# Kernel tuning notes

Measured on AMD Instinct MI355X. Metric: run time of the kernel, lower is better.

## Reference

```python
import jax, jax.numpy as jnp
import numpy as np

NW, NT, ND = 100000, 20000, 5000      # wallet / token / dev node counts
DW, DT, DD = 32, 32, 16               # raw feature dims
H = 64                                 # GATConv out channels (heads=1)
E_WW, E_BU, E_SE, E_CR = 1600000, 1000000, 1000000, 20000


def setup_inputs() -> dict:
    key = jax.random.key(0)
    ks = iter(jax.random.split(key, 80))

    def nrm(shape, s=1.0):
        return jax.random.normal(next(ks), shape, dtype=jnp.float32) * s

    inp = {
        "x_wallet": nrm((NW, DW)),
        "x_token": nrm((NT, DT)),
        "x_dev": nrm((ND, DD)),
    }
    # per-relation GATConv params: lin_src, lin_dst (bias=False), att_src, att_dst, bias
    rels = [("g1ww", DW, DW), ("g1bu", DW, DT), ("g1se", DW, DT), ("g1cr", DD, DT),
            ("g2ww", H, H), ("g2bu", H, H), ("g2se", H, H)]
    for pre, ds, dd in rels:
        inp[pre + "_Ws"] = nrm((ds, H), 0.1)
        inp[pre + "_Wd"] = nrm((dd, H), 0.1)
        inp[pre + "_as"] = nrm((H,), 0.1)
        inp[pre + "_ad"] = nrm((H,), 0.1)
        inp[pre + "_b"] = nrm((H,), 0.1)
    inp["Wfc"] = nrm((H, 2), 0.1)
    inp["bfc"] = nrm((2,), 0.1)

    for name, n, hi in [("ww_src", E_WW, NW), ("ww_dst", E_WW, NW),
                        ("bu_src", E_BU, NW), ("bu_dst", E_BU, NT),
                        ("se_src", E_SE, NW), ("se_dst", E_SE, NT),
                        ("cr_src", E_CR, ND), ("cr_dst", E_CR, NT)]:
        inp[name] = jax.random.randint(next(ks), (n,), 0, hi, dtype=jnp.int32)
    return inp


def gat(xs, xd, src, dst, Ws, Wd, a_s, a_d, b, n_dst):
    """PyG GATConv, heads=1, add_self_loops=False, negative_slope=0.2."""
    hs = xs @ Ws                                   # [Ns, H]
    e = jax.nn.leaky_relu((hs @ a_s)[src] + ((xd @ Wd) @ a_d)[dst], 0.2)  # [E]
    m = jax.ops.segment_max(e, dst, num_segments=n_dst)
    ex = jnp.exp(e - m[dst])
    den = jax.ops.segment_sum(ex, dst, num_segments=n_dst)
    alpha = ex / (den[dst] + 1e-16)                # scatter-softmax over dst
    out = jax.ops.segment_sum(alpha[:, None] * hs[src], dst, num_segments=n_dst)
    return out + b


def reference(x_wallet, x_token, x_dev,
              g1ww_Ws, g1ww_Wd, g1ww_as, g1ww_ad, g1ww_b,
              g1bu_Ws, g1bu_Wd, g1bu_as, g1bu_ad, g1bu_b,
              g1se_Ws, g1se_Wd, g1se_as, g1se_ad, g1se_b,
              g1cr_Ws, g1cr_Wd, g1cr_as, g1cr_ad, g1cr_b,
              g2ww_Ws, g2ww_Wd, g2ww_as, g2ww_ad, g2ww_b,
              g2bu_Ws, g2bu_Wd, g2bu_as, g2bu_ad, g2bu_b,
              g2se_Ws, g2se_Wd, g2se_as, g2se_ad, g2se_b,
              Wfc, bfc,
              ww_src, ww_dst, bu_src, bu_dst, se_src, se_dst, cr_src, cr_dst):
    # conv1 (HeteroConv, aggr='sum'): dev has no incoming edges -> dropped
    w1 = gat(x_wallet, x_wallet, ww_src, ww_dst, g1ww_Ws, g1ww_Wd, g1ww_as, g1ww_ad, g1ww_b, NW)
    t1 = (gat(x_wallet, x_token, bu_src, bu_dst, g1bu_Ws, g1bu_Wd, g1bu_as, g1bu_ad, g1bu_b, NT)
          + gat(x_wallet, x_token, se_src, se_dst, g1se_Ws, g1se_Wd, g1se_as, g1se_ad, g1se_b, NT)
          + gat(x_dev, x_token, cr_src, cr_dst, g1cr_Ws, g1cr_Wd, g1cr_as, g1cr_ad, g1cr_b, NT))
    # conv2: 'dev' absent from x_dict, so ('dev','creates','token') is skipped by HeteroConv
    w2 = gat(w1, w1, ww_src, ww_dst, g2ww_Ws, g2ww_Wd, g2ww_as, g2ww_ad, g2ww_b, NW)  # computed but unused downstream (matches torch)
    t2 = (gat(w1, t1, bu_src, bu_dst, g2bu_Ws, g2bu_Wd, g2bu_as, g2bu_ad, g2bu_b, NT)
          + gat(w1, t1, se_src, se_dst, g2se_Ws, g2se_Wd, g2se_as, g2se_ad, g2se_b, NT))
    del w2
    return t2 @ Wfc + bfc  # [NT, 2]
```

## Files before the change

kernel.cpp:

```cpp
#include <hip/hip_runtime.h>

#define NW 100000
#define NT 20000
#define ND 5000
#define EWW 1600000
#define EBU 1000000
#define ESE 1000000
#define ECR 20000
#define EPB 16384
#define BTH 512

#define WWSH 8
#define WWW 256
#define NBWB 391
#define WCAP 6144
#define TSH 6
#define TW 64
#define NBTB 313
#define TCAP 4096
#define CCAP 512

typedef unsigned int uint;

#define R_EDWW 0
#define R_EDBU 1
#define R_EDSE 2
#define R_EDCR 3
#define R_WV2BU 4
#define R_WV2SE 5
#define R_ESWW 6
#define R_ESBU 7
#define R_ESSE 8
#define R_ESCR 9
#define R_WS2BU 10
#define R_WS2SE 11
#define R_VBU 12
#define R_VSE 13
#define R_DBU_B 14
#define R_DSE_B 15
#define R_DBU_S 16
#define R_DSE_S 17
#define R_DBU_C 18
#define R_DSE_C 19
#define R_TBU0 20
#define R_TBU1 21
#define R_TSE0 22
#define R_TSE1 23
#define R_CBU 24
#define R_CSE 25
#define R_SBU 26
#define R_SSE 27
#define R_MBU0 28
#define R_MBU1 29
#define R_MSE0 30
#define R_MSE1 31
#define R_CB1U0 32
#define R_CB1U1 33
#define R_CB1S0 34
#define R_CB1S1 35
#define R_C20 36
#define R_C21 37
#define R_F0 38
#define R_F1 39
#define R_BT1 40
#define R_BT2 41
#define NROWS 42


__global__ void k_scur(int* __restrict__ ccur) {
    int t = blockIdx.x * 256 + threadIdx.x;
    if (t < 4096) {
        int li = t >> 10, i = t & 1023;
        int cap = (li == 0) ? WCAP : (li == 3 ? CCAP : TCAP);
        ccur[t] = i * cap;
    }
}

__global__ __launch_bounds__(64) void k_bsum(const float* __restrict__ b0,
                                             const float* __restrict__ b1,
                                             const float* __restrict__ b2,
                                             float* __restrict__ out) {
    int t = threadIdx.x;
    float v = b0[t] + b1[t];
    if (b2) v += b2[t];
    out[t] = v;
}

__global__ __launch_bounds__(64) void k_prepfc(const float* __restrict__ Wfc,
                                               float* __restrict__ f0,
                                               float* __restrict__ f1) {
    int t = threadIdx.x;
    f0[t] = Wfc[t * 2];
    f1[t] = Wfc[t * 2 + 1];
}


struct BMeta {
    const int* src[4]; const int* dst[4];
    int* ccur[4];
    uint* pairs[4];
    int E[4]; int shift[4]; int cap[4]; int bbase[5];
};

__device__ __forceinline__ int find_list(const int* bbase, int b) {
    int li = 0;
    while (li < 3 && b >= bbase[li + 1]) ++li;
    return li;
}

__global__ __launch_bounds__(BTH) void k_cscat4(BMeta a) {
    __shared__ int scnt[1024];
    __shared__ int sbase[1024];
    for (int i = threadIdx.x; i < 1024; i += BTH) scnt[i] = 0;
    __syncthreads();
    int li = find_list(a.bbase, blockIdx.x);
    int lb = blockIdx.x - a.bbase[li];
    const int* src = a.src[li];
    const int* dst = a.dst[li];
    uint* pairs = a.pairs[li];
    int* ccur = a.ccur[li];
    int sh = a.shift[li];
    int cap = a.cap[li];
    uint mask = (1u << sh) - 1u;
    int b0 = lb * EPB;
    int end = min(b0 + EPB, a.E[li]);
    for (int i = b0 + threadIdx.x; i < end; i += BTH)
        atomicAdd(&scnt[dst[i] >> sh], 1);
    __syncthreads();
    for (int i = threadIdx.x; i < 1024; i += BTH) {
        int c = scnt[i];
        sbase[i] = c ? atomicAdd(&ccur[i], c) : 0;
        scnt[i] = 0;
    }
    __syncthreads();
    for (int i = b0 + threadIdx.x; i < end; i += BTH) {
        int d = dst[i];
        int b = d >> sh;
        int p = sbase[b] + atomicAdd(&scnt[b], 1);
        if (p < (b + 1) * cap)
            pairs[p] = (uint)src[i] | (((uint)d & mask) << 20);
    }
}


struct WvN { const float* M[16]; const float* v[16]; int K[16]; };

__global__ __launch_bounds__(64) void k_wvN(WvN a, float* __restrict__ out) {
    int b = blockIdx.x, t = threadIdx.x;
    if (t < a.K[b]) {
        const float* M = a.M[b];
        const float* v = a.v[b];
        float s = 0.f;
        for (int j = 0; j < 64; ++j) s = fmaf(M[t * 64 + j], v[j], s);
        out[b * 64 + t] = s;
    }
}


struct PrepWP {
    const float* X; int N;
    const float* v[14];
    float* esww; float* esbu; float* esse; float* edww;
    float* P6; float2* Pbu; float2* Pse;
};

__global__ __launch_bounds__(256) void k_prepw(PrepWP a) {
    int wvid = (blockIdx.x * 256 + threadIdx.x) >> 6;
    int half = (threadIdx.x >> 5) & 1;
    int l = threadIdx.x & 31;
    int r = wvid * 2 + half;
    float x = (r < a.N) ? a.X[(size_t)r * 32 + l] : 0.f;
    float p[14];
#pragma unroll
    for (int i = 0; i < 14; ++i) p[i] = x * a.v[i][l];
#pragma unroll
    for (int o = 1; o < 32; o <<= 1) {
#pragma unroll
        for (int i = 0; i < 14; ++i) p[i] += __shfl_xor(p[i], o, 64);
    }
    if (l == 0 && r < a.N) {
        a.esww[r] = p[0]; a.esbu[r] = p[1]; a.esse[r] = p[2]; a.edww[r] = p[3];
        float4* P = (float4*)(a.P6 + (size_t)r * 8);
        P[0] = make_float4(p[4], p[5], p[6], p[7]);
        P[1] = make_float4(p[8], p[9], 0.f, 0.f);
        a.Pbu[r] = make_float2(p[10], p[11]);
        a.Pse[r] = make_float2(p[12], p[13]);
    }
}

struct PrepTD {
    const float* Xt; const float* Xd;
    const float* tv0; const float* tv1; const float* tv2;
    const float* dv0; const float* dv1; const float* dv2;
    float* e0; float* e1; float* e2;
    float* escr; float2* Pcr;
    int nbT;
};

__global__ __launch_bounds__(256) void k_preptd(PrepTD a) {
    if ((int)blockIdx.x < a.nbT) {
        int wvid = (blockIdx.x * 256 + threadIdx.x) >> 6;
        int half = (threadIdx.x >> 5) & 1;
        int l = threadIdx.x & 31;
        int r = wvid * 2 + half;
        float x = (r < NT) ? a.Xt[(size_t)r * 32 + l] : 0.f;
        float p0 = x * a.tv0[l], p1 = x * a.tv1[l], p2 = x * a.tv2[l];
#pragma unroll
        for (int o = 1; o < 32; o <<= 1) {
            p0 += __shfl_xor(p0, o, 64);
            p1 += __shfl_xor(p1, o, 64);
            p2 += __shfl_xor(p2, o, 64);
        }
        if (l == 0 && r < NT) { a.e0[r] = p0; a.e1[r] = p1; a.e2[r] = p2; }
    } else {
        int grp = ((blockIdx.x - a.nbT) * 256 + threadIdx.x) >> 4;
        int l = threadIdx.x & 15;
        int r = grp;
        float x = (r < ND) ? a.Xd[(size_t)r * 16 + l] : 0.f;
        float p0 = x * a.dv0[l], p1 = x * a.dv1[l], p2 = x * a.dv2[l];
#pragma unroll
        for (int o = 1; o < 16; o <<= 1) {
            p0 += __shfl_xor(p0, o, 64);
            p1 += __shfl_xor(p1, o, 64);
            p2 += __shfl_xor(p2, o, 64);
        }
        if (l == 0 && r < ND) { a.escr[r] = p0; a.Pcr[r] = make_float2(p1, p2); }
    }
}


__device__ __forceinline__ void sort_bucket(const uint* __restrict__ slab, int cnt,
                                            int ndl, uint* sp, int* hoff, int* hcnt,
                                            int t) {
    if (t < ndl) hcnt[t] = 0;
    __syncthreads();
    for (int i = t; i < cnt; i += BTH) atomicAdd(&hcnt[slab[i] >> 20], 1);
    __syncthreads();
    int own = (t < ndl) ? hcnt[t] : 0;
    if (t < ndl) hoff[t] = own;
    __syncthreads();
    for (int o = 1; o < ndl; o <<= 1) {
        int u = 0;
        if (t < ndl && t >= o) u = hoff[t - o];
        __syncthreads();
        if (t < ndl && t >= o) hoff[t] += u;
        __syncthreads();
    }
    if (t < ndl) { hoff[t] -= own; hcnt[t] = 0; }
    __syncthreads();
    for (int i = t; i < cnt; i += BTH) {
        uint pr = slab[i];
        int g = pr >> 20;
        int pos = hoff[g] + atomicAdd(&hcnt[g], 1);
        sp[pos] = pr & 0xFFFFFu;
    }
    __syncthreads();
}


__global__ __launch_bounds__(BTH) void k_fsaggw(const uint* __restrict__ pairs,
                                                const int* __restrict__ ccur,
                                                const float* __restrict__ es,
                                                const float* __restrict__ ed,
                                                const float* __restrict__ P6,
                                                const float* __restrict__ C,
                                                float* __restrict__ es2bu,
                                                float* __restrict__ es2se,
                                                float2* __restrict__ Pl2bu,
                                                float2* __restrict__ Pl2se) {
    __shared__ uint sp[WCAP];
    __shared__ int hoff[WWW];
    __shared__ int hcnt[WWW];
    __shared__ float eds[WWW];
    int t = threadIdx.x, b = blockIdx.x;
    int d0 = b << WWSH;
    if (t < WWW) {
        int d = d0 + t;
        eds[t] = (d < NW) ? ed[d] : 0.f;
    }
    int cnt = min(ccur[b] - b * WCAP, WCAP);
    sort_bucket(pairs + (size_t)b * WCAP, cnt, WWW, sp, hoff, hcnt, t);
    int dl = t >> 1, sub = t & 1;
    float edj = eds[dl];
    float A0 = 0, A1 = 0, A2 = 0, A3 = 0, A4 = 0, A5 = 0, den = 0;
    int s0 = hoff[dl], s1 = s0 + hcnt[dl];
    for (int j = s0 + sub; j < s1; j += 2) {
        int s = sp[j];
        float e = es[s] + edj;
        e = e > 0.f ? e : 0.2f * e;
        float w = __expf(e);
        const float4* P = (const float4*)(P6 + (size_t)s * 8);
        float4 u = P[0], v = P[1];
        den += w;
        A0 = fmaf(w, u.x, A0); A1 = fmaf(w, u.y, A1); A2 = fmaf(w, u.z, A2);
        A3 = fmaf(w, u.w, A3); A4 = fmaf(w, v.x, A4); A5 = fmaf(w, v.y, A5);
    }
    A0 += __shfl_xor(A0, 1, 64); A1 += __shfl_xor(A1, 1, 64);
    A2 += __shfl_xor(A2, 1, 64); A3 += __shfl_xor(A3, 1, 64);
    A4 += __shfl_xor(A4, 1, 64); A5 += __shfl_xor(A5, 1, 64);
    den += __shfl_xor(den, 1, 64);
    if (sub == 0) {
        int d = d0 + dl;
        if (d < NW) {
            float c0 = C[R_CBU * 64], c1 = C[R_CSE * 64];
            float c2 = C[R_CB1U0 * 64], c3 = C[R_CB1U1 * 64];
            float c4 = C[R_CB1S0 * 64], c5 = C[R_CB1S1 * 64];
            if (den > 0.f) {
                float inv = 1.f / (den + 1e-16f);
                es2bu[d] = A0 * inv + c0;
                es2se[d] = A1 * inv + c1;
                Pl2bu[d] = make_float2(A2 * inv + c2, A3 * inv + c3);
                Pl2se[d] = make_float2(A4 * inv + c4, A5 * inv + c5);
            } else {
                es2bu[d] = c0;
                es2se[d] = c1;
                Pl2bu[d] = make_float2(c2, c3);
                Pl2se[d] = make_float2(c4, c5);
            }
        }
    }
}


__global__ __launch_bounds__(BTH) void k_fsaggt(const uint* __restrict__ pB,
                                                const uint* __restrict__ pS,
                                                const uint* __restrict__ pC,
                                                const int* __restrict__ curB,
                                                const int* __restrict__ curS,
                                                const int* __restrict__ curC,
                                                const float* __restrict__ esB,
                                                const float* __restrict__ esS,
                                                const float* __restrict__ esC,
                                                const float* __restrict__ edB,
                                                const float* __restrict__ edS,
                                                const float* __restrict__ edC,
                                                const float2* __restrict__ PB,
                                                const float2* __restrict__ PS,
                                                const float2* __restrict__ PC,
                                                const float* __restrict__ es2bu,
                                                const float* __restrict__ es2se,
                                                const float2* __restrict__ Pl2bu,
                                                const float2* __restrict__ Pl2se,
                                                const float* __restrict__ C,
                                                const float* __restrict__ bfc,
                                                float* __restrict__ out) {
    __shared__ uint spB[TCAP];
    __shared__ uint spS[TCAP];
    __shared__ uint spC[CCAP];
    __shared__ int hoB[TW], hcB[TW], hoS[TW], hcS[TW], hoC[TW], hcC[TW];
    __shared__ float eds[3][TW];
    int t = threadIdx.x, b = blockIdx.x;
    int d0 = b << TSH;
    if (t < TW) {
        int d = d0 + t;
        eds[0][t] = (d < NT) ? edB[d] : 0.f;
        eds[1][t] = (d < NT) ? edS[d] : 0.f;
        eds[2][t] = (d < NT) ? edC[d] : 0.f;
    }
    int cntB = min(curB[b] - b * TCAP, TCAP);
    int cntS = min(curS[b] - b * TCAP, TCAP);
    int cntC = min(curC[b] - b * CCAP, CCAP);
    sort_bucket(pB + (size_t)b * TCAP, cntB, TW, spB, hoB, hcB, t);
    sort_bucket(pS + (size_t)b * TCAP, cntS, TW, spS, hoS, hcS, t);
    sort_bucket(pC + (size_t)b * CCAP, cntC, TW, spC, hoC, hcC, t);

    int dl = t >> 3, sub = t & 7;

    float bx = 0, by = 0, bd = 0;
    for (int j = hoB[dl] + sub; j < hoB[dl] + hcB[dl]; j += 8) {
        int s = spB[j];
        float e = esB[s] + eds[0][dl];
        e = e > 0.f ? e : 0.2f * e;
        float w = __expf(e);
        float2 p = PB[s];
        bd += w; bx = fmaf(w, p.x, bx); by = fmaf(w, p.y, by);
    }
    float sx = 0, sy = 0, sd = 0;
    for (int j = hoS[dl] + sub; j < hoS[dl] + hcS[dl]; j += 8) {
        int s = spS[j];
        float e = esS[s] + eds[1][dl];
        e = e > 0.f ? e : 0.2f * e;
        float w = __expf(e);
        float2 p = PS[s];
        sd += w; sx = fmaf(w, p.x, sx); sy = fmaf(w, p.y, sy);
    }
    float cx = 0, cy = 0, cd = 0;
    for (int j = hoC[dl] + sub; j < hoC[dl] + hcC[dl]; j += 8) {
        int s = spC[j];
        float e = esC[s] + eds[2][dl];
        e = e > 0.f ? e : 0.2f * e;
        float w = __expf(e);
        float2 p = PC[s];
        cd += w; cx = fmaf(w, p.x, cx); cy = fmaf(w, p.y, cy);
    }
#pragma unroll
    for (int o = 1; o < 8; o <<= 1) {
        bx += __shfl_xor(bx, o, 64); by += __shfl_xor(by, o, 64); bd += __shfl_xor(bd, o, 64);
        sx += __shfl_xor(sx, o, 64); sy += __shfl_xor(sy, o, 64); sd += __shfl_xor(sd, o, 64);
        cx += __shfl_xor(cx, o, 64); cy += __shfl_xor(cy, o, 64); cd += __shfl_xor(cd, o, 64);
    }
    float qbx = 0, qby = 0, qsx = 0, qsy = 0, qcx = 0, qcy = 0;
    if (bd > 0.f) { float i = 1.f / (bd + 1e-16f); qbx = bx * i; qby = by * i; }
    if (sd > 0.f) { float i = 1.f / (sd + 1e-16f); qsx = sx * i; qsy = sy * i; }
    if (cd > 0.f) { float i = 1.f / (cd + 1e-16f); qcx = cx * i; qcy = cy * i; }
    float ed2b = C[R_SBU * 64] + qbx + qsx + qcx;
    float ed2s = C[R_SSE * 64] + qby + qsy + qcy;

    float rbx = 0, rby = 0, rbd = 0;
    for (int j = hoB[dl] + sub; j < hoB[dl] + hcB[dl]; j += 8) {
        int s = spB[j];
        float e = es2bu[s] + ed2b;
        e = e > 0.f ? e : 0.2f * e;
        float w = __expf(e);
        float2 p = Pl2bu[s];
        rbd += w; rbx = fmaf(w, p.x, rbx); rby = fmaf(w, p.y, rby);
    }
    float rsx = 0, rsy = 0, rsd = 0;
    for (int j = hoS[dl] + sub; j < hoS[dl] + hcS[dl]; j += 8) {
        int s = spS[j];
        float e = es2se[s] + ed2s;
        e = e > 0.f ? e : 0.2f * e;
        float w = __expf(e);
        float2 p = Pl2se[s];
        rsd += w; rsx = fmaf(w, p.x, rsx); rsy = fmaf(w, p.y, rsy);
    }
#pragma unroll
    for (int o = 1; o < 8; o <<= 1) {
        rbx += __shfl_xor(rbx, o, 64); rby += __shfl_xor(rby, o, 64); rbd += __shfl_xor(rbd, o, 64);
        rsx += __shfl_xor(rsx, o, 64); rsy += __shfl_xor(rsy, o, 64); rsd += __shfl_xor(rsd, o, 64);
    }
    if (sub == 0) {
        int d = d0 + dl;
        if (d < NT) {
            float fbx = 0, fby = 0, fsx = 0, fsy = 0;
            if (rbd > 0.f) { float i = 1.f / (rbd + 1e-16f); fbx = rbx * i; fby = rby * i; }
            if (rsd > 0.f) { float i = 1.f / (rsd + 1e-16f); fsx = rsx * i; fsy = rsy * i; }
            out[d * 2 + 0] = bfc[0] + C[R_C20 * 64] + fbx + fsx;
            out[d * 2 + 1] = bfc[1] + C[R_C21 * 64] + fby + fsy;
        }
    }
}


extern "C" void kernel_launch(void* const* d_in, const int* in_sizes, int n_in,
                              void* d_out, int out_size, void* d_ws, size_t ws_size,
                              hipStream_t stream) {
    const float* xw = (const float*)d_in[0];
    const float* xt = (const float*)d_in[1];
    const float* xd = (const float*)d_in[2];
    const float* g1ww_Ws = (const float*)d_in[3];
    const float* g1ww_Wd = (const float*)d_in[4];
    const float* g1ww_as = (const float*)d_in[5];
    const float* g1ww_ad = (const float*)d_in[6];
    const float* g1ww_b  = (const float*)d_in[7];
    const float* g1bu_Ws = (const float*)d_in[8];
    const float* g1bu_Wd = (const float*)d_in[9];
    const float* g1bu_as = (const float*)d_in[10];
    const float* g1bu_ad = (const float*)d_in[11];
    const float* g1bu_b  = (const float*)d_in[12];
    const float* g1se_Ws = (const float*)d_in[13];
    const float* g1se_Wd = (const float*)d_in[14];
    const float* g1se_as = (const float*)d_in[15];
    const float* g1se_ad = (const float*)d_in[16];
    const float* g1se_b  = (const float*)d_in[17];
    const float* g1cr_Ws = (const float*)d_in[18];
    const float* g1cr_Wd = (const float*)d_in[19];
    const float* g1cr_as = (const float*)d_in[20];
    const float* g1cr_ad = (const float*)d_in[21];
    const float* g1cr_b  = (const float*)d_in[22];
    const float* g2bu_Ws = (const float*)d_in[28];
    const float* g2bu_Wd = (const float*)d_in[29];
    const float* g2bu_as = (const float*)d_in[30];
    const float* g2bu_ad = (const float*)d_in[31];
    const float* g2bu_b  = (const float*)d_in[32];
    const float* g2se_Ws = (const float*)d_in[33];
    const float* g2se_Wd = (const float*)d_in[34];
    const float* g2se_as = (const float*)d_in[35];
    const float* g2se_ad = (const float*)d_in[36];
    const float* g2se_b  = (const float*)d_in[37];
    const float* Wfc = (const float*)d_in[38];
    const float* bfc = (const float*)d_in[39];
    const int* ww_src = (const int*)d_in[40];
    const int* ww_dst = (const int*)d_in[41];
    const int* bu_src = (const int*)d_in[42];
    const int* bu_dst = (const int*)d_in[43];
    const int* se_src = (const int*)d_in[44];
    const int* se_dst = (const int*)d_in[45];
    const int* cr_src = (const int*)d_in[46];
    const int* cr_dst = (const int*)d_in[47];

    char* p = (char*)d_ws;
    auto alloc = [&](size_t bytes) {
        char* r = p;
        p += (bytes + 255) & ~(size_t)255;
        return r;
    };
    uint* pairsW = (uint*)alloc((size_t)NBWB * WCAP * 4);
    uint* pairsB = (uint*)alloc((size_t)NBTB * TCAP * 4);
    uint* pairsS = (uint*)alloc((size_t)NBTB * TCAP * 4);
    uint* pairsC = (uint*)alloc((size_t)NBTB * CCAP * 4);
    int* ccur = (int*)alloc(4 * 1024 * 4);

    float* wvbuf = (float*)alloc(NROWS * 64 * 4);

    float* esww = (float*)alloc((size_t)NW * 4);
    float* esbu = (float*)alloc((size_t)NW * 4);
    float* esse = (float*)alloc((size_t)NW * 4);
    float* edww = (float*)alloc((size_t)NW * 4);
    float* edbu = (float*)alloc((size_t)NT * 4);
    float* edse = (float*)alloc((size_t)NT * 4);
    float* edcr = (float*)alloc((size_t)NT * 4);
    float* escr = (float*)alloc((size_t)ND * 4);
    float* P6   = (float*)alloc((size_t)NW * 8 * 4);
    float2* Pbu = (float2*)alloc((size_t)NW * 8);
    float2* Pse = (float2*)alloc((size_t)NW * 8);
    float2* Pcr = (float2*)alloc((size_t)ND * 8);
    float* es2bu = (float*)alloc((size_t)NW * 4);
    float* es2se = (float*)alloc((size_t)NW * 4);
    float2* Pl2bu = (float2*)alloc((size_t)NW * 8);
    float2* Pl2se = (float2*)alloc((size_t)NW * 8);

    const int thr = 256;
    const int nbW_e = (EWW + EPB - 1) / EPB;
    const int nbB_e = (EBU + EPB - 1) / EPB;
    const int nbS_e = (ESE + EPB - 1) / EPB;
    const int nbC_e = (ECR + EPB - 1) / EPB;
    const int nbTot = nbW_e + nbB_e + nbS_e + nbC_e;

    k_scur<<<16, thr, 0, stream>>>(ccur);

    BMeta bm;
    bm.src[0] = ww_src; bm.dst[0] = ww_dst; bm.ccur[0] = ccur + 0 * 1024;
    bm.pairs[0] = pairsW; bm.E[0] = EWW; bm.shift[0] = WWSH; bm.cap[0] = WCAP;
    bm.src[1] = bu_src; bm.dst[1] = bu_dst; bm.ccur[1] = ccur + 1 * 1024;
    bm.pairs[1] = pairsB; bm.E[1] = EBU; bm.shift[1] = TSH; bm.cap[1] = TCAP;
    bm.src[2] = se_src; bm.dst[2] = se_dst; bm.ccur[2] = ccur + 2 * 1024;
    bm.pairs[2] = pairsS; bm.E[2] = ESE; bm.shift[2] = TSH; bm.cap[2] = TCAP;
    bm.src[3] = cr_src; bm.dst[3] = cr_dst; bm.ccur[3] = ccur + 3 * 1024;
    bm.pairs[3] = pairsC; bm.E[3] = ECR; bm.shift[3] = TSH; bm.cap[3] = CCAP;
    bm.bbase[0] = 0; bm.bbase[1] = nbW_e; bm.bbase[2] = nbW_e + nbB_e;
    bm.bbase[3] = nbW_e + nbB_e + nbS_e; bm.bbase[4] = nbTot;
    k_cscat4<<<nbTot, BTH, 0, stream>>>(bm);

    k_prepfc<<<1, 64, 0, stream>>>(Wfc, wvbuf + R_F0 * 64, wvbuf + R_F1 * 64);
    k_bsum<<<1, 64, 0, stream>>>(g1bu_b, g1se_b, g1cr_b, wvbuf + R_BT1 * 64);
    k_bsum<<<1, 64, 0, stream>>>(g2bu_b, g2se_b, nullptr, wvbuf + R_BT2 * 64);

    WvN A;
    A.M[0] = g1ww_Wd; A.v[0] = g1ww_ad; A.K[0] = 32;
    A.M[1] = g1bu_Wd; A.v[1] = g1bu_ad; A.K[1] = 32;
    A.M[2] = g1se_Wd; A.v[2] = g1se_ad; A.K[2] = 32;
    A.M[3] = g1cr_Wd; A.v[3] = g1cr_ad; A.K[3] = 32;
    A.M[4] = g2bu_Wd; A.v[4] = g2bu_ad; A.K[4] = 64;
    A.M[5] = g2se_Wd; A.v[5] = g2se_ad; A.K[5] = 64;
    A.M[6] = g1ww_Ws; A.v[6] = g1ww_as; A.K[6] = 32;
    A.M[7] = g1bu_Ws; A.v[7] = g1bu_as; A.K[7] = 32;
    A.M[8] = g1se_Ws; A.v[8] = g1se_as; A.K[8] = 32;
    A.M[9] = g1cr_Ws; A.v[9] = g1cr_as; A.K[9] = 16;
    A.M[10] = g2bu_Ws; A.v[10] = g2bu_as; A.K[10] = 64;
    A.M[11] = g2se_Ws; A.v[11] = g2se_as; A.K[11] = 64;
    for (int i = 12; i < 16; ++i) { A.M[i] = nullptr; A.v[i] = nullptr; A.K[i] = 0; }
    k_wvN<<<12, 64, 0, stream>>>(A, wvbuf + 0 * 64);

    WvN B;
    B.M[0] = g1ww_Ws; B.v[0] = wvbuf + R_WS2BU * 64; B.K[0] = 32;
    B.M[1] = g1ww_Ws; B.v[1] = wvbuf + R_WS2SE * 64; B.K[1] = 32;
    B.M[2] = g1bu_Ws; B.v[2] = wvbuf + R_WV2BU * 64; B.K[2] = 32;
    B.M[3] = g1bu_Ws; B.v[3] = wvbuf + R_WV2SE * 64; B.K[3] = 32;
    B.M[4] = g1se_Ws; B.v[4] = wvbuf + R_WV2BU * 64; B.K[4] = 32;
    B.M[5] = g1se_Ws; B.v[5] = wvbuf + R_WV2SE * 64; B.K[5] = 32;
    B.M[6] = g1cr_Ws; B.v[6] = wvbuf + R_WV2BU * 64; B.K[6] = 16;
    B.M[7] = g1cr_Ws; B.v[7] = wvbuf + R_WV2SE * 64; B.K[7] = 16;
    B.M[8] = g2bu_Ws; B.v[8] = wvbuf + R_F0 * 64; B.K[8] = 64;
    B.M[9] = g2bu_Ws; B.v[9] = wvbuf + R_F1 * 64; B.K[9] = 64;
    B.M[10] = g2se_Ws; B.v[10] = wvbuf + R_F0 * 64; B.K[10] = 64;
    B.M[11] = g2se_Ws; B.v[11] = wvbuf + R_F1 * 64; B.K[11] = 64;
    B.M[12] = g1ww_b; B.v[12] = wvbuf + R_WS2BU * 64; B.K[12] = 1;
    B.M[13] = g1ww_b; B.v[13] = wvbuf + R_WS2SE * 64; B.K[13] = 1;
    B.M[14] = wvbuf + R_BT1 * 64; B.v[14] = wvbuf + R_WV2BU * 64; B.K[14] = 1;
    B.M[15] = wvbuf + R_BT1 * 64; B.v[15] = wvbuf + R_WV2SE * 64; B.K[15] = 1;
    k_wvN<<<16, 64, 0, stream>>>(B, wvbuf + R_VBU * 64);

    WvN Cc;
    Cc.M[0] = g1ww_Ws; Cc.v[0] = wvbuf + R_TBU0 * 64; Cc.K[0] = 32;
    Cc.M[1] = g1ww_Ws; Cc.v[1] = wvbuf + R_TBU1 * 64; Cc.K[1] = 32;
    Cc.M[2] = g1ww_Ws; Cc.v[2] = wvbuf + R_TSE0 * 64; Cc.K[2] = 32;
    Cc.M[3] = g1ww_Ws; Cc.v[3] = wvbuf + R_TSE1 * 64; Cc.K[3] = 32;
    Cc.M[4] = g1ww_b; Cc.v[4] = wvbuf + R_TBU0 * 64; Cc.K[4] = 1;
    Cc.M[5] = g1ww_b; Cc.v[5] = wvbuf + R_TBU1 * 64; Cc.K[5] = 1;
    Cc.M[6] = g1ww_b; Cc.v[6] = wvbuf + R_TSE0 * 64; Cc.K[6] = 1;
    Cc.M[7] = g1ww_b; Cc.v[7] = wvbuf + R_TSE1 * 64; Cc.K[7] = 1;
    Cc.M[8] = wvbuf + R_BT2 * 64; Cc.v[8] = wvbuf + R_F0 * 64; Cc.K[8] = 1;
    Cc.M[9] = wvbuf + R_BT2 * 64; Cc.v[9] = wvbuf + R_F1 * 64; Cc.K[9] = 1;
    for (int i = 10; i < 16; ++i) { Cc.M[i] = nullptr; Cc.v[i] = nullptr; Cc.K[i] = 0; }
    k_wvN<<<10, 64, 0, stream>>>(Cc, wvbuf + R_MBU0 * 64);

    PrepWP pw;
    pw.X = xw; pw.N = NW;
    pw.v[0] = wvbuf + R_ESWW * 64; pw.v[1] = wvbuf + R_ESBU * 64;
    pw.v[2] = wvbuf + R_ESSE * 64; pw.v[3] = wvbuf + R_EDWW * 64;
    pw.v[4] = wvbuf + R_VBU * 64;  pw.v[5] = wvbuf + R_VSE * 64;
    pw.v[6] = wvbuf + R_MBU0 * 64; pw.v[7] = wvbuf + R_MBU1 * 64;
    pw.v[8] = wvbuf + R_MSE0 * 64; pw.v[9] = wvbuf + R_MSE1 * 64;
    pw.v[10] = wvbuf + R_DBU_B * 64; pw.v[11] = wvbuf + R_DSE_B * 64;
    pw.v[12] = wvbuf + R_DBU_S * 64; pw.v[13] = wvbuf + R_DSE_S * 64;
    pw.esww = esww; pw.esbu = esbu; pw.esse = esse; pw.edww = edww;
    pw.P6 = P6; pw.Pbu = Pbu; pw.Pse = Pse;
    k_prepw<<<(NW + 7) / 8, thr, 0, stream>>>(pw);

    PrepTD ptd;
    ptd.Xt = xt; ptd.Xd = xd;
    ptd.tv0 = wvbuf + R_EDBU * 64; ptd.tv1 = wvbuf + R_EDSE * 64; ptd.tv2 = wvbuf + R_EDCR * 64;
    ptd.dv0 = wvbuf + R_ESCR * 64; ptd.dv1 = wvbuf + R_DBU_C * 64; ptd.dv2 = wvbuf + R_DSE_C * 64;
    ptd.e0 = edbu; ptd.e1 = edse; ptd.e2 = edcr;
    ptd.escr = escr; ptd.Pcr = Pcr;
    ptd.nbT = (NT + 7) / 8;
    k_preptd<<<ptd.nbT + (ND + 15) / 16, thr, 0, stream>>>(ptd);

    k_fsaggw<<<NBWB, BTH, 0, stream>>>(pairsW, ccur + 0 * 1024, esww, edww, P6, wvbuf,
                                       es2bu, es2se, Pl2bu, Pl2se);

    k_fsaggt<<<NBTB, BTH, 0, stream>>>(pairsB, pairsS, pairsC,
                                       ccur + 1 * 1024, ccur + 2 * 1024, ccur + 3 * 1024,
                                       esbu, esse, escr, edbu, edse, edcr,
                                       Pbu, Pse, Pcr,
                                       es2bu, es2se, Pl2bu, Pl2se,
                                       wvbuf, bfc, (float*)d_out);
}
```

Before: 326.0 us.

## Double block threads, widen per-destination lanes, merge tiny prep kernels

Raises the block size from 512 to 1024 threads, which applies to the bucket-scatter kernel and, implicitly, to the aggregation kernels whose lane mapping now assumes 4 lanes per wallet destination and 16 per token destination. The wider split lets more threads work through each destination's edge list, which suits skewed in-degrees, at the cost of extra shuffle reduction steps. Three one-block setup kernels are merged into one 3-block launch to cut launch overhead. The risks are lower occupancy and register pressure at 1024 threads, and the need for every affected kernel to actually be launched with 1024 threads.

```diff
diff --git a/kernel.cpp b/kernel.cpp
--- a/kernel.cpp
+++ b/kernel.cpp
@@ -8,7 +8,7 @@
 #define ESE 1000000
 #define ECR 20000
 #define EPB 16384
-#define BTH 512
+#define BTH 1024
 
 #define WWSH 8
 #define WWW 256
@@ -76,22 +76,22 @@
     }
 }
 
-__global__ __launch_bounds__(64) void k_bsum(const float* __restrict__ b0,
-                                             const float* __restrict__ b1,
-                                             const float* __restrict__ b2,
-                                             float* __restrict__ out) {
+__global__ __launch_bounds__(64) void k_smallprep(const float* __restrict__ Wfc,
+                                                  const float* __restrict__ b1a,
+                                                  const float* __restrict__ b1b,
+                                                  const float* __restrict__ b1c,
+                                                  const float* __restrict__ b2a,
+                                                  const float* __restrict__ b2b,
+                                                  float* __restrict__ wvbuf) {
     int t = threadIdx.x;
-    float v = b0[t] + b1[t];
-    if (b2) v += b2[t];
-    out[t] = v;
-}
-
-__global__ __launch_bounds__(64) void k_prepfc(const float* __restrict__ Wfc,
-                                               float* __restrict__ f0,
-                                               float* __restrict__ f1) {
-    int t = threadIdx.x;
-    f0[t] = Wfc[t * 2];
-    f1[t] = Wfc[t * 2 + 1];
+    if (blockIdx.x == 0) {
+        wvbuf[R_F0 * 64 + t] = Wfc[t * 2];
+        wvbuf[R_F1 * 64 + t] = Wfc[t * 2 + 1];
+    } else if (blockIdx.x == 1) {
+        wvbuf[R_BT1 * 64 + t] = b1a[t] + b1b[t] + b1c[t];
+    } else {
+        wvbuf[R_BT2 * 64 + t] = b2a[t] + b2b[t];
+    }
 }
 
 
@@ -280,11 +280,11 @@
     }
     int cnt = min(ccur[b] - b * WCAP, WCAP);
     sort_bucket(pairs + (size_t)b * WCAP, cnt, WWW, sp, hoff, hcnt, t);
-    int dl = t >> 1, sub = t & 1;
+    int dl = t >> 2, sub = t & 3;
     float edj = eds[dl];
     float A0 = 0, A1 = 0, A2 = 0, A3 = 0, A4 = 0, A5 = 0, den = 0;
     int s0 = hoff[dl], s1 = s0 + hcnt[dl];
-    for (int j = s0 + sub; j < s1; j += 2) {
+    for (int j = s0 + sub; j < s1; j += 4) {
         int s = sp[j];
         float e = es[s] + edj;
         e = e > 0.f ? e : 0.2f * e;
@@ -295,10 +295,13 @@
         A0 = fmaf(w, u.x, A0); A1 = fmaf(w, u.y, A1); A2 = fmaf(w, u.z, A2);
         A3 = fmaf(w, u.w, A3); A4 = fmaf(w, v.x, A4); A5 = fmaf(w, v.y, A5);
     }
-    A0 += __shfl_xor(A0, 1, 64); A1 += __shfl_xor(A1, 1, 64);
-    A2 += __shfl_xor(A2, 1, 64); A3 += __shfl_xor(A3, 1, 64);
-    A4 += __shfl_xor(A4, 1, 64); A5 += __shfl_xor(A5, 1, 64);
-    den += __shfl_xor(den, 1, 64);
+#pragma unroll
+    for (int o = 1; o < 4; o <<= 1) {
+        A0 += __shfl_xor(A0, o, 64); A1 += __shfl_xor(A1, o, 64);
+        A2 += __shfl_xor(A2, o, 64); A3 += __shfl_xor(A3, o, 64);
+        A4 += __shfl_xor(A4, o, 64); A5 += __shfl_xor(A5, o, 64);
+        den += __shfl_xor(den, o, 64);
+    }
     if (sub == 0) {
         int d = d0 + dl;
         if (d < NW) {
@@ -364,10 +367,10 @@
     sort_bucket(pS + (size_t)b * TCAP, cntS, TW, spS, hoS, hcS, t);
     sort_bucket(pC + (size_t)b * CCAP, cntC, TW, spC, hoC, hcC, t);
 
-    int dl = t >> 3, sub = t & 7;
+    int dl = t >> 4, sub = t & 15;
 
     float bx = 0, by = 0, bd = 0;
-    for (int j = hoB[dl] + sub; j < hoB[dl] + hcB[dl]; j += 8) {
+    for (int j = hoB[dl] + sub; j < hoB[dl] + hcB[dl]; j += 16) {
         int s = spB[j];
         float e = esB[s] + eds[0][dl];
         e = e > 0.f ? e : 0.2f * e;
@@ -376,7 +379,7 @@
         bd += w; bx = fmaf(w, p.x, bx); by = fmaf(w, p.y, by);
     }
     float sx = 0, sy = 0, sd = 0;
-    for (int j = hoS[dl] + sub; j < hoS[dl] + hcS[dl]; j += 8) {
+    for (int j = hoS[dl] + sub; j < hoS[dl] + hcS[dl]; j += 16) {
         int s = spS[j];
         float e = esS[s] + eds[1][dl];
         e = e > 0.f ? e : 0.2f * e;
@@ -385,7 +388,7 @@
         sd += w; sx = fmaf(w, p.x, sx); sy = fmaf(w, p.y, sy);
     }
     float cx = 0, cy = 0, cd = 0;
-    for (int j = hoC[dl] + sub; j < hoC[dl] + hcC[dl]; j += 8) {
+    for (int j = hoC[dl] + sub; j < hoC[dl] + hcC[dl]; j += 16) {
         int s = spC[j];
         float e = esC[s] + eds[2][dl];
         e = e > 0.f ? e : 0.2f * e;
@@ -394,7 +397,7 @@
         cd += w; cx = fmaf(w, p.x, cx); cy = fmaf(w, p.y, cy);
     }
 #pragma unroll
-    for (int o = 1; o < 8; o <<= 1) {
+    for (int o = 1; o < 16; o <<= 1) {
         bx += __shfl_xor(bx, o, 64); by += __shfl_xor(by, o, 64); bd += __shfl_xor(bd, o, 64);
         sx += __shfl_xor(sx, o, 64); sy += __shfl_xor(sy, o, 64); sd += __shfl_xor(sd, o, 64);
         cx += __shfl_xor(cx, o, 64); cy += __shfl_xor(cy, o, 64); cd += __shfl_xor(cd, o, 64);
@@ -407,7 +410,7 @@
     float ed2s = C[R_SSE * 64] + qby + qsy + qcy;
 
     float rbx = 0, rby = 0, rbd = 0;
-    for (int j = hoB[dl] + sub; j < hoB[dl] + hcB[dl]; j += 8) {
+    for (int j = hoB[dl] + sub; j < hoB[dl] + hcB[dl]; j += 16) {
         int s = spB[j];
         float e = es2bu[s] + ed2b;
         e = e > 0.f ? e : 0.2f * e;
@@ -416,7 +419,7 @@
         rbd += w; rbx = fmaf(w, p.x, rbx); rby = fmaf(w, p.y, rby);
     }
     float rsx = 0, rsy = 0, rsd = 0;
-    for (int j = hoS[dl] + sub; j < hoS[dl] + hcS[dl]; j += 8) {
+    for (int j = hoS[dl] + sub; j < hoS[dl] + hcS[dl]; j += 16) {
         int s = spS[j];
         float e = es2se[s] + ed2s;
         e = e > 0.f ? e : 0.2f * e;
@@ -425,7 +428,7 @@
         rsd += w; rsx = fmaf(w, p.x, rsx); rsy = fmaf(w, p.y, rsy);
     }
 #pragma unroll
-    for (int o = 1; o < 8; o <<= 1) {
+    for (int o = 1; o < 16; o <<= 1) {
         rbx += __shfl_xor(rbx, o, 64); rby += __shfl_xor(rby, o, 64); rbd += __shfl_xor(rbd, o, 64);
         rsx += __shfl_xor(rsx, o, 64); rsy += __shfl_xor(rsy, o, 64); rsd += __shfl_xor(rsd, o, 64);
     }
@@ -542,9 +545,7 @@
     bm.bbase[3] = nbW_e + nbB_e + nbS_e; bm.bbase[4] = nbTot;
     k_cscat4<<<nbTot, BTH, 0, stream>>>(bm);
 
-    k_prepfc<<<1, 64, 0, stream>>>(Wfc, wvbuf + R_F0 * 64, wvbuf + R_F1 * 64);
-    k_bsum<<<1, 64, 0, stream>>>(g1bu_b, g1se_b, g1cr_b, wvbuf + R_BT1 * 64);
-    k_bsum<<<1, 64, 0, stream>>>(g2bu_b, g2se_b, nullptr, wvbuf + R_BT2 * 64);
+    k_smallprep<<<3, 64, 0, stream>>>(Wfc, g1bu_b, g1se_b, g1cr_b, g2bu_b, g2se_b, wvbuf);
 
     WvN A;
     A.M[0] = g1ww_Wd; A.v[0] = g1ww_ad; A.K[0] = 32;
```

New measurement: 338.8 us. 1.04x slower.
